# Performance work log

Measured on AMD Instinct MI355X. Metric: run time of the kernel, lower is better.

Reference implementation:

```python
import jax, jax.numpy as jnp
import numpy as np

M, N = 4096, 4096  # placement density grid size (even, as the rfft-based kernel assumes)


def _expk(L):
    # precompute_expk(L): [cos(pi*k/(2L)), sin(pi*k/(2L))] stacked -> [L, 2]
    a = np.pi * np.arange(L) / (2.0 * L)
    return np.stack([np.cos(a), np.sin(a)], axis=-1).astype(np.float32)


def setup_inputs() -> dict:
    key = jax.random.key(0)
    x = jax.random.normal(key, (M, N), dtype=jnp.float32)
    return {
        "x": x,
        "expkM": jnp.asarray(_expk(M)),
        "expkN": jnp.asarray(_expk(N)),
    }


def _idct1d(x, expk):
    # Unnormalized IDCT (DCT-III with DC weight 1) along the last axis:
    #   y_u = sum_k x_k * cos(pi*k*(2u+1)/(2L))
    # Makhoul FFT trick: c_k = x_k * exp(i*pi*k/(2L)); v = L*ifft(c);
    #   y[2m] = Re(v[m]),  y[2m+1] = Re(v[L-1-m])
    L = x.shape[-1]
    ek = expk[:, 0] + 1j * expk[:, 1]            # exp(i*pi*k/(2L)), [L]
    v = (jnp.fft.ifft(x * ek, axis=-1) * L).real  # [..., L]
    half = L // 2
    even = v[..., :half]                          # y[0], y[2], ...
    odd = v[..., ::-1][..., :half]                # y[1], y[3], ... (= v[L-1], v[L-2], ...)
    return jnp.stack([even, odd], axis=-1).reshape(x.shape)


def reference(x, expkM, expkN):
    # out[u,v] = sum_{p,q} x[p,q] cos(pi*p*(2u+1)/(2M)) cos(pi*q*(2v+1)/(2N))
    t = _idct1d(x, expkN)                               # transform along N (last dim)
    out = _idct1d(t.swapaxes(-1, -2), expkM)            # transform along M
    return out.swapaxes(-1, -2)
```

## Files before the change

### kernel.cpp

```cpp
#include <hip/hip_runtime.h>
#include <stdint.h>

typedef __bf16 bf16x8_t __attribute__((ext_vector_type(8)));
typedef float f32x4_t __attribute__((ext_vector_type(4)));

__device__ __forceinline__ uint32_t f32_to_bf16_bits(float f) {
    union { float f; uint32_t u; } v; v.f = f;
    return (v.u + 0x7FFFu + ((v.u >> 16) & 1u)) >> 16;
}

__global__ void prep_kernel(const float* __restrict__ X,
                            unsigned short* __restrict__ Ae,
                            unsigned short* __restrict__ Ao,
                            unsigned short* __restrict__ Xe,
                            unsigned short* __restrict__ Xo) {
    if (blockIdx.x < 4096) {
        const int idx = blockIdx.x * 256 + threadIdx.x;
        const int sel = idx >> 19;
        const int e   = idx & ((1 << 19) - 1);
        const int n   = e >> 8;
        const int c0  = (e & 255) << 3;
        const uint32_t tn = (uint32_t)(2 * n + 1);
        unsigned short* dst = sel ? Ao : Ae;
        uint32_t packed[4];
#pragma unroll
        for (int jj = 0; jj < 4; ++jj) {
            uint32_t cA = (uint32_t)(c0 + 2 * jj);
            uint32_t cB = cA + 1;
            uint32_t r0 = ((2u * cA + (uint32_t)sel) * tn) & 16383u;
            uint32_t r1 = ((2u * cB + (uint32_t)sel) * tn) & 16383u;
            float v0 = __cosf((float)r0 * 3.8349519697141e-4f);
            float v1 = __cosf((float)r1 * 3.8349519697141e-4f);
            packed[jj] = f32_to_bf16_bits(v0) | (f32_to_bf16_bits(v1) << 16);
        }
        *(uint4*)(dst + (size_t)n * 2048 + c0) = make_uint4(packed[0], packed[1], packed[2], packed[3]);
    } else {
        const int idx = (blockIdx.x - 4096) * 256 + threadIdx.x;
        const int q   = idx >> 9;
        const int p0  = (idx & 511) << 3;
        const float4* src = (const float4*)(X + (size_t)q * 4096 + p0);
        float4 a = src[0];
        float4 b = src[1];
        uint2 ev, od;
        ev.x = f32_to_bf16_bits(a.x) | (f32_to_bf16_bits(a.z) << 16);
        ev.y = f32_to_bf16_bits(b.x) | (f32_to_bf16_bits(b.z) << 16);
        od.x = f32_to_bf16_bits(a.y) | (f32_to_bf16_bits(a.w) << 16);
        od.y = f32_to_bf16_bits(b.y) | (f32_to_bf16_bits(b.w) << 16);
        *(uint2*)(Xe + (size_t)q * 2048 + (p0 >> 1)) = ev;
        *(uint2*)(Xo + (size_t)q * 2048 + (p0 >> 1)) = od;
    }
}

template <int STAGE>
__global__ __launch_bounds__(256, 2)
void gemm_fused_kernel(const unsigned short* __restrict__ Ae,
                       const unsigned short* __restrict__ Ao,
                       const unsigned short* __restrict__ Re,
                       const unsigned short* __restrict__ Ro,
                       unsigned short* __restrict__ Te,
                       unsigned short* __restrict__ To,
                       float* __restrict__ out) {
    constexpr int KD = 2048;
    constexpr int BK = 64;
    __shared__ __attribute__((aligned(16))) unsigned short lAe[128 * BK];
    __shared__ __attribute__((aligned(16))) unsigned short lAo[128 * BK];
    __shared__ __attribute__((aligned(16))) unsigned short lBe[128 * BK];
    __shared__ __attribute__((aligned(16))) unsigned short lBo[128 * BK];

    const int tid  = threadIdx.x;
    const int wave = tid >> 6;
    const int lane = tid & 63;

    const int tile_m = blockIdx.y << 7;
    const int tile_c = blockIdx.x << 7;

    f32x4_t acc_e[4][4], acc_o[4][4];
#pragma unroll
    for (int i = 0; i < 4; ++i)
#pragma unroll
        for (int j = 0; j < 4; ++j) {
            acc_e[i][j] = (f32x4_t){0.f, 0.f, 0.f, 0.f};
            acc_o[i][j] = (f32x4_t){0.f, 0.f, 0.f, 0.f};
        }

    const int c_base = wave << 6;
    size_t roff[4];
#pragma unroll
    for (int t = 0; t < 4; ++t) {
        const int cl   = c_base + lane + 256 * t;
        const int row  = cl >> 3;
        const int grp  = (cl & 7) ^ (row & 7);
        roff[t] = (size_t)row * KD + ((size_t)grp << 3);
    }

    const unsigned short* gAe = Ae + (size_t)tile_m * KD;
    const unsigned short* gAo = Ao + (size_t)tile_m * KD;
    const unsigned short* gBe = Re + (size_t)tile_c * KD;
    const unsigned short* gBo = Ro + (size_t)tile_c * KD;

    int lbase[4];
#pragma unroll
    for (int t = 0; t < 4; ++t) lbase[t] = (c_base + 256 * t) << 3;

    const int frow = lane & 15;
    const int sw   = frow & 7;
    const int gq   = lane >> 4;
    const int aRowB = ((wave >> 1) * 64 + frow) * BK;
    const int bRowB = ((wave & 1) * 64 + frow) * BK;

#define GLL(gp, lp) __builtin_amdgcn_global_load_lds( \
        (const __attribute__((address_space(1))) uint32_t*)(gp), \
        (__attribute__((address_space(3))) uint32_t*)(lp), 16, 0, 0)

    for (int kt = 0; kt < KD / BK; ++kt) {
        const size_t kadv = (size_t)kt * BK;
        __syncthreads();
#pragma unroll
        for (int t = 0; t < 4; ++t) {
            GLL(gAe + kadv + roff[t], &lAe[lbase[t]]);
            GLL(gAo + kadv + roff[t], &lAo[lbase[t]]);
            GLL(gBe + kadv + roff[t], &lBe[lbase[t]]);
            GLL(gBo + kadv + roff[t], &lBo[lbase[t]]);
        }
        __syncthreads();

#pragma unroll
        for (int kh = 0; kh < 2; ++kh) {
            const int slotOff = (((kh * 4 + gq) ^ sw) << 3);
            {
                bf16x8_t af[4], bfr[4];
#pragma unroll
                for (int i = 0; i < 4; ++i) af[i]  = *(const bf16x8_t*)(&lAe[aRowB + i * 16 * BK + slotOff]);
#pragma unroll
                for (int j = 0; j < 4; ++j) bfr[j] = *(const bf16x8_t*)(&lBe[bRowB + j * 16 * BK + slotOff]);
#pragma unroll
                for (int i = 0; i < 4; ++i)
#pragma unroll
                    for (int j = 0; j < 4; ++j)
                        acc_e[i][j] = __builtin_amdgcn_mfma_f32_16x16x32_bf16(af[i], bfr[j], acc_e[i][j], 0, 0, 0);
            }
            {
                bf16x8_t af[4], bfr[4];
#pragma unroll
                for (int i = 0; i < 4; ++i) af[i]  = *(const bf16x8_t*)(&lAo[aRowB + i * 16 * BK + slotOff]);
#pragma unroll
                for (int j = 0; j < 4; ++j) bfr[j] = *(const bf16x8_t*)(&lBo[bRowB + j * 16 * BK + slotOff]);
#pragma unroll
                for (int i = 0; i < 4; ++i)
#pragma unroll
                    for (int j = 0; j < 4; ++j)
                        acc_o[i][j] = __builtin_amdgcn_mfma_f32_16x16x32_bf16(af[i], bfr[j], acc_o[i][j], 0, 0, 0);
            }
        }
    }
#undef GLL

    const int orow = tile_m + (wave >> 1) * 64 + ((lane >> 4) << 2);
    const int ocol = tile_c + (wave & 1) * 64 + (lane & 15);
    if (STAGE == 1) {
        unsigned short* dst = (ocol & 1) ? To : Te;
#pragma unroll
        for (int i = 0; i < 4; ++i)
#pragma unroll
            for (int j = 0; j < 4; ++j)
#pragma unroll
                for (int r = 0; r < 4; ++r) {
                    const int n = orow + i * 16 + r;
                    const int c = (ocol + j * 16) >> 1;
                    const float e = acc_e[i][j][r], o = acc_o[i][j][r];
                    dst[(size_t)n * 2048 + c]          = (unsigned short)f32_to_bf16_bits(e + o);
                    dst[(size_t)(4095 - n) * 2048 + c] = (unsigned short)f32_to_bf16_bits(e - o);
                }
    } else {
#pragma unroll
        for (int i = 0; i < 4; ++i)
#pragma unroll
            for (int j = 0; j < 4; ++j)
#pragma unroll
                for (int r = 0; r < 4; ++r) {
                    const int m = orow + i * 16 + r;
                    const int w = ocol + j * 16;
                    const float e = acc_e[i][j][r], o = acc_o[i][j][r];
                    out[(size_t)m * 4096 + w]          = e + o;
                    out[(size_t)(4095 - m) * 4096 + w] = e - o;
                }
    }
}

extern "C" void kernel_launch(void* const* d_in, const int* in_sizes, int n_in,
                              void* d_out, int out_size, void* d_ws, size_t ws_size,
                              hipStream_t stream) {
    const float* x = (const float*)d_in[0];
    char* ws = (char*)d_ws;
    const size_t MB = 1024 * 1024;
    unsigned short* Ae = (unsigned short*)(ws);
    unsigned short* Ao = (unsigned short*)(ws + 8 * MB);
    unsigned short* Xe = (unsigned short*)(ws + 16 * MB);
    unsigned short* Xo = (unsigned short*)(ws + 32 * MB);
    unsigned short* Te = (unsigned short*)(ws + 48 * MB);
    unsigned short* To = (unsigned short*)(ws + 64 * MB);
    float* out = (float*)d_out;

    prep_kernel<<<12288, 256, 0, stream>>>(x, Ae, Ao, Xe, Xo);

    dim3 grid(32, 16);
    gemm_fused_kernel<1><<<grid, 256, 0, stream>>>(Ae, Ao, Xe, Xo, Te, To, nullptr);
    gemm_fused_kernel<2><<<grid, 256, 0, stream>>>(Ae, Ao, Te, To, nullptr, nullptr, out);
}
```

Before: 252.9 us.

## Triple-buffer LDS with interleaved async loads and 8-wave 128x256 tiles

```diff
diff --git a/kernel.cpp b/kernel.cpp
--- a/kernel.cpp
+++ b/kernel.cpp
@@ -51,8 +51,72 @@
     }
 }
 
+#define GLL(gp, lp) __builtin_amdgcn_global_load_lds( \
+        (const __attribute__((address_space(1))) uint32_t*)(gp), \
+        (__attribute__((address_space(3))) uint32_t*)(lp), 16, 0, 0)
+
+template <bool PRE, int VM>
+__device__ __forceinline__ void tile_step(f32x4_t (&acc)[4][4], const int t,
+        int& cur_off, int& stg_off, unsigned short* smem,
+        const unsigned short* pAe, const unsigned short* pAo,
+        const unsigned short* pBe, const unsigned short* pBo,
+        const int* a_src, const int* b_src, const int* a_lds, const int* b_lds,
+        const int aRow, const int bRow, const int gq, const int sw) {
+    const unsigned short* gA = pAe;
+    const unsigned short* gB = pBe;
+    size_t kadv = 0;
+    if (PRE) {
+        const int pre = t + 2;
+        gA = (pre < 32) ? pAe : pAo;
+        gB = (pre < 32) ? pBe : pBo;
+        kadv = (size_t)(pre & 31) << 6;
+    }
+    unsigned short* sA = smem + stg_off;
+    unsigned short* sB = sA + 8192;
+    const unsigned short* lA = smem + cur_off;
+    const unsigned short* lB = lA + 8192;
+
+#pragma unroll
+    for (int kh = 0; kh < 2; ++kh) {
+        const int so = (((kh << 2) + gq) ^ sw) << 3;
+        bf16x8_t af[4], bfr[4];
+#pragma unroll
+        for (int i = 0; i < 4; ++i) af[i]  = *(const bf16x8_t*)(lA + aRow + i * 1024 + so);
+#pragma unroll
+        for (int j = 0; j < 4; ++j) bfr[j] = *(const bf16x8_t*)(lB + bRow + j * 1024 + so);
+        if (PRE) {
+            if (kh == 0) {
+                GLL(gA + kadv + a_src[0], sA + a_lds[0]);
+                GLL(gB + kadv + b_src[0], sB + b_lds[0]);
+                GLL(gB + kadv + b_src[1], sB + b_lds[1]);
+            } else {
+                GLL(gA + kadv + a_src[1], sA + a_lds[1]);
+                GLL(gB + kadv + b_src[2], sB + b_lds[2]);
+                GLL(gB + kadv + b_src[3], sB + b_lds[3]);
+            }
+        }
+        asm volatile("" ::: "memory");
+        __builtin_amdgcn_s_barrier();
+        __builtin_amdgcn_s_setprio(1);
+#pragma unroll
+        for (int i = 0; i < 4; ++i)
+#pragma unroll
+            for (int j = 0; j < 4; ++j)
+                acc[i][j] = __builtin_amdgcn_mfma_f32_16x16x32_bf16(af[i], bfr[j], acc[i][j], 0, 0, 0);
+        __builtin_amdgcn_s_setprio(0);
+        if (kh == 1) {
+            if (VM == 6)      asm volatile("s_waitcnt vmcnt(6)" ::: "memory");
+            else if (VM == 0) asm volatile("s_waitcnt vmcnt(0)" ::: "memory");
+        }
+        asm volatile("" ::: "memory");
+        __builtin_amdgcn_s_barrier();
+    }
+    cur_off += 24576; if (cur_off == 73728) cur_off = 0;
+    stg_off += 24576; if (stg_off == 73728) stg_off = 0;
+}
+
 template <int STAGE>
-__global__ __launch_bounds__(256, 2)
+__global__ __launch_bounds__(512, 2)
 void gemm_fused_kernel(const unsigned short* __restrict__ Ae,
                        const unsigned short* __restrict__ Ao,
                        const unsigned short* __restrict__ Re,
@@ -61,18 +125,21 @@
                        unsigned short* __restrict__ To,
                        float* __restrict__ out) {
     constexpr int KD = 2048;
-    constexpr int BK = 64;
-    __shared__ __attribute__((aligned(16))) unsigned short lAe[128 * BK];
-    __shared__ __attribute__((aligned(16))) unsigned short lAo[128 * BK];
-    __shared__ __attribute__((aligned(16))) unsigned short lBe[128 * BK];
-    __shared__ __attribute__((aligned(16))) unsigned short lBo[128 * BK];
+    __shared__ __attribute__((aligned(16))) unsigned short smem[3 * 24576];
 
     const int tid  = threadIdx.x;
     const int wave = tid >> 6;
     const int lane = tid & 63;
-
-    const int tile_m = blockIdx.y << 7;
-    const int tile_c = blockIdx.x << 7;
+    const int wm   = wave >> 2;
+    const int wn   = wave & 3;
+
+    const int tile_n = blockIdx.y << 7;
+    const int tile_c = blockIdx.x << 8;
+
+    const unsigned short* pAe = Ae + (size_t)tile_n * KD;
+    const unsigned short* pAo = Ao + (size_t)tile_n * KD;
+    const unsigned short* pBe = Re + (size_t)tile_c * KD;
+    const unsigned short* pBo = Ro + (size_t)tile_c * KD;
 
     f32x4_t acc_e[4][4], acc_o[4][4];
 #pragma unroll
@@ -83,90 +150,73 @@
             acc_o[i][j] = (f32x4_t){0.f, 0.f, 0.f, 0.f};
         }
 
-    const int c_base = wave << 6;
-    size_t roff[4];
-#pragma unroll
-    for (int t = 0; t < 4; ++t) {
-        const int cl   = c_base + lane + 256 * t;
-        const int row  = cl >> 3;
-        const int grp  = (cl & 7) ^ (row & 7);
-        roff[t] = (size_t)row * KD + ((size_t)grp << 3);
-    }
-
-    const unsigned short* gAe = Ae + (size_t)tile_m * KD;
-    const unsigned short* gAo = Ao + (size_t)tile_m * KD;
-    const unsigned short* gBe = Re + (size_t)tile_c * KD;
-    const unsigned short* gBo = Ro + (size_t)tile_c * KD;
-
-    int lbase[4];
-#pragma unroll
-    for (int t = 0; t < 4; ++t) lbase[t] = (c_base + 256 * t) << 3;
+    int a_src[2], a_lds[2], b_src[4], b_lds[4];
+#pragma unroll
+    for (int k2 = 0; k2 < 2; ++k2) {
+        const int c = tid + 512 * k2, row = c >> 3, g = (c & 7) ^ (row & 7);
+        a_src[k2] = row * KD + g * 8;
+        a_lds[k2] = c * 8;
+    }
+#pragma unroll
+    for (int k2 = 0; k2 < 4; ++k2) {
+        const int c = tid + 512 * k2, row = c >> 3, g = (c & 7) ^ (row & 7);
+        b_src[k2] = row * KD + g * 8;
+        b_lds[k2] = c * 8;
+    }
 
     const int frow = lane & 15;
     const int sw   = frow & 7;
     const int gq   = lane >> 4;
-    const int aRowB = ((wave >> 1) * 64 + frow) * BK;
-    const int bRowB = ((wave & 1) * 64 + frow) * BK;
-
-#define GLL(gp, lp) __builtin_amdgcn_global_load_lds( \
-        (const __attribute__((address_space(1))) uint32_t*)(gp), \
-        (__attribute__((address_space(3))) uint32_t*)(lp), 16, 0, 0)
-
-    for (int kt = 0; kt < KD / BK; ++kt) {
-        const size_t kadv = (size_t)kt * BK;
-        __syncthreads();
-#pragma unroll
-        for (int t = 0; t < 4; ++t) {
-            GLL(gAe + kadv + roff[t], &lAe[lbase[t]]);
-            GLL(gAo + kadv + roff[t], &lAo[lbase[t]]);
-            GLL(gBe + kadv + roff[t], &lBe[lbase[t]]);
-            GLL(gBo + kadv + roff[t], &lBo[lbase[t]]);
-        }
-        __syncthreads();
-
-#pragma unroll
-        for (int kh = 0; kh < 2; ++kh) {
-            const int slotOff = (((kh * 4 + gq) ^ sw) << 3);
-            {
-                bf16x8_t af[4], bfr[4];
-#pragma unroll
-                for (int i = 0; i < 4; ++i) af[i]  = *(const bf16x8_t*)(&lAe[aRowB + i * 16 * BK + slotOff]);
-#pragma unroll
-                for (int j = 0; j < 4; ++j) bfr[j] = *(const bf16x8_t*)(&lBe[bRowB + j * 16 * BK + slotOff]);
-#pragma unroll
-                for (int i = 0; i < 4; ++i)
-#pragma unroll
-                    for (int j = 0; j < 4; ++j)
-                        acc_e[i][j] = __builtin_amdgcn_mfma_f32_16x16x32_bf16(af[i], bfr[j], acc_e[i][j], 0, 0, 0);
-            }
-            {
-                bf16x8_t af[4], bfr[4];
-#pragma unroll
-                for (int i = 0; i < 4; ++i) af[i]  = *(const bf16x8_t*)(&lAo[aRowB + i * 16 * BK + slotOff]);
-#pragma unroll
-                for (int j = 0; j < 4; ++j) bfr[j] = *(const bf16x8_t*)(&lBo[bRowB + j * 16 * BK + slotOff]);
-#pragma unroll
-                for (int i = 0; i < 4; ++i)
-#pragma unroll
-                    for (int j = 0; j < 4; ++j)
-                        acc_o[i][j] = __builtin_amdgcn_mfma_f32_16x16x32_bf16(af[i], bfr[j], acc_o[i][j], 0, 0, 0);
-            }
-        }
-    }
-#undef GLL
-
-    const int orow = tile_m + (wave >> 1) * 64 + ((lane >> 4) << 2);
-    const int ocol = tile_c + (wave & 1) * 64 + (lane & 15);
+    const int aRow = (wm * 64 + frow) * 64;
+    const int bRow = (wn * 64 + frow) * 64;
+
+    {
+        unsigned short* s0 = smem;
+        GLL(pAe + a_src[0], s0 + a_lds[0]);
+        GLL(pBe + b_src[0], s0 + 8192 + b_lds[0]);
+        GLL(pBe + b_src[1], s0 + 8192 + b_lds[1]);
+        GLL(pAe + a_src[1], s0 + a_lds[1]);
+        GLL(pBe + b_src[2], s0 + 8192 + b_lds[2]);
+        GLL(pBe + b_src[3], s0 + 8192 + b_lds[3]);
+        unsigned short* s1 = smem + 24576;
+        GLL(pAe + 64 + a_src[0], s1 + a_lds[0]);
+        GLL(pBe + 64 + b_src[0], s1 + 8192 + b_lds[0]);
+        GLL(pBe + 64 + b_src[1], s1 + 8192 + b_lds[1]);
+        GLL(pAe + 64 + a_src[1], s1 + a_lds[1]);
+        GLL(pBe + 64 + b_src[2], s1 + 8192 + b_lds[2]);
+        GLL(pBe + 64 + b_src[3], s1 + 8192 + b_lds[3]);
+        asm volatile("s_waitcnt vmcnt(6)" ::: "memory");
+        __builtin_amdgcn_s_barrier();
+    }
+
+    int cur_off = 0;
+    int stg_off = 49152;
+
+#pragma unroll 1
+    for (int t = 0; t < 32; ++t)
+        tile_step<true, 6>(acc_e, t, cur_off, stg_off, smem, pAe, pAo, pBe, pBo,
+                           a_src, b_src, a_lds, b_lds, aRow, bRow, gq, sw);
+#pragma unroll 1
+    for (int t = 32; t < 62; ++t)
+        tile_step<true, 6>(acc_o, t, cur_off, stg_off, smem, pAe, pAo, pBe, pBo,
+                           a_src, b_src, a_lds, b_lds, aRow, bRow, gq, sw);
+    tile_step<false, 0>(acc_o, 62, cur_off, stg_off, smem, pAe, pAo, pBe, pBo,
+                        a_src, b_src, a_lds, b_lds, aRow, bRow, gq, sw);
+    tile_step<false, -1>(acc_o, 63, cur_off, stg_off, smem, pAe, pAo, pBe, pBo,
+                         a_src, b_src, a_lds, b_lds, aRow, bRow, gq, sw);
+
+    const int orow0 = tile_n + wm * 64 + ((lane >> 4) << 2);
+    const int ocol0 = tile_c + wn * 64 + (lane & 15);
     if (STAGE == 1) {
-        unsigned short* dst = (ocol & 1) ? To : Te;
+        unsigned short* dst = (ocol0 & 1) ? To : Te;
 #pragma unroll
         for (int i = 0; i < 4; ++i)
 #pragma unroll
             for (int j = 0; j < 4; ++j)
 #pragma unroll
                 for (int r = 0; r < 4; ++r) {
-                    const int n = orow + i * 16 + r;
-                    const int c = (ocol + j * 16) >> 1;
+                    const int n = orow0 + i * 16 + r;
+                    const int c = (ocol0 + j * 16) >> 1;
                     const float e = acc_e[i][j][r], o = acc_o[i][j][r];
                     dst[(size_t)n * 2048 + c]          = (unsigned short)f32_to_bf16_bits(e + o);
                     dst[(size_t)(4095 - n) * 2048 + c] = (unsigned short)f32_to_bf16_bits(e - o);
@@ -178,8 +228,8 @@
             for (int j = 0; j < 4; ++j)
 #pragma unroll
                 for (int r = 0; r < 4; ++r) {
-                    const int m = orow + i * 16 + r;
-                    const int w = ocol + j * 16;
+                    const int m = orow0 + i * 16 + r;
+                    const int w = ocol0 + j * 16;
                     const float e = acc_e[i][j][r], o = acc_o[i][j][r];
                     out[(size_t)m * 4096 + w]          = e + o;
                     out[(size_t)(4095 - m) * 4096 + w] = e - o;
@@ -203,7 +253,7 @@
 
     prep_kernel<<<12288, 256, 0, stream>>>(x, Ae, Ao, Xe, Xo);
 
-    dim3 grid(32, 16);
-    gemm_fused_kernel<1><<<grid, 256, 0, stream>>>(Ae, Ao, Xe, Xo, Te, To, nullptr);
-    gemm_fused_kernel<2><<<grid, 256, 0, stream>>>(Ae, Ao, Te, To, nullptr, nullptr, out);
-}
+    dim3 grid(16, 16);
+    gemm_fused_kernel<1><<<grid, 512, 0, stream>>>(Ae, Ao, Xe, Xo, Te, To, nullptr);
+    gemm_fused_kernel<2><<<grid, 512, 0, stream>>>(Ae, Ao, Te, To, nullptr, nullptr, out);
+}
```

Measured after the change: 265.8 us. +5.1%, slower.

## Double-buffer LDS and stream even then odd K-phases to overlap loads with MFMA

Applied to the files above, without the earlier changes.

```diff
diff --git a/kernel.cpp b/kernel.cpp
--- a/kernel.cpp
+++ b/kernel.cpp
@@ -51,6 +51,45 @@
     }
 }
 
+#define GLL(gp, lp) __builtin_amdgcn_global_load_lds( \
+        (const __attribute__((address_space(1))) uint32_t*)(gp), \
+        (__attribute__((address_space(3))) uint32_t*)(lp), 16, 0, 0)
+
+#define STAGE8(buf, gA, gB, kadv) do {                                        \
+    _Pragma("unroll")                                                         \
+    for (int k_ = 0; k_ < 4; ++k_) {                                          \
+        GLL((gA) + (kadv) + src_off[k_], (buf) + uldsb[k_]);                  \
+        GLL((gB) + (kadv) + src_off[k_], (buf) + 8192 + uldsb[k_]);           \
+    }                                                                         \
+} while (0)
+
+#define COMPUTE_TILE(buf, acc) do {                                           \
+    const unsigned short* lA_ = (buf);                                        \
+    const unsigned short* lB_ = (buf) + 8192;                                 \
+    _Pragma("unroll")                                                         \
+    for (int kh_ = 0; kh_ < 2; ++kh_) {                                       \
+        const int so_ = (((kh_ << 2) + gq) ^ sw) << 3;                        \
+        bf16x8_t af_[4], bf_[4];                                              \
+        _Pragma("unroll")                                                     \
+        for (int i_ = 0; i_ < 4; ++i_) af_[i_] = *(const bf16x8_t*)(lA_ + aRow + i_ * 1024 + so_); \
+        _Pragma("unroll")                                                     \
+        for (int j_ = 0; j_ < 4; ++j_) bf_[j_] = *(const bf16x8_t*)(lB_ + bRow + j_ * 1024 + so_); \
+        __builtin_amdgcn_s_setprio(1);                                        \
+        _Pragma("unroll")                                                     \
+        for (int i_ = 0; i_ < 4; ++i_)                                        \
+            _Pragma("unroll")                                                 \
+            for (int j_ = 0; j_ < 4; ++j_)                                    \
+                acc[i_][j_] = __builtin_amdgcn_mfma_f32_16x16x32_bf16(af_[i_], bf_[j_], acc[i_][j_], 0, 0, 0); \
+        __builtin_amdgcn_s_setprio(0);                                        \
+    }                                                                         \
+} while (0)
+
+#define TILE_SYNC() do {                                                      \
+    asm volatile("s_waitcnt vmcnt(0)" ::: "memory");                          \
+    __builtin_amdgcn_s_barrier();                                             \
+    asm volatile("" ::: "memory");                                            \
+} while (0)
+
 template <int STAGE>
 __global__ __launch_bounds__(256, 2)
 void gemm_fused_kernel(const unsigned short* __restrict__ Ae,
@@ -61,11 +100,7 @@
                        unsigned short* __restrict__ To,
                        float* __restrict__ out) {
     constexpr int KD = 2048;
-    constexpr int BK = 64;
-    __shared__ __attribute__((aligned(16))) unsigned short lAe[128 * BK];
-    __shared__ __attribute__((aligned(16))) unsigned short lAo[128 * BK];
-    __shared__ __attribute__((aligned(16))) unsigned short lBe[128 * BK];
-    __shared__ __attribute__((aligned(16))) unsigned short lBo[128 * BK];
+    __shared__ __attribute__((aligned(16))) unsigned short smem[2 * 16384];
 
     const int tid  = threadIdx.x;
     const int wave = tid >> 6;
@@ -73,6 +108,11 @@
 
     const int tile_m = blockIdx.y << 7;
     const int tile_c = blockIdx.x << 7;
+
+    const unsigned short* pAe = Ae + (size_t)tile_m * KD;
+    const unsigned short* pAo = Ao + (size_t)tile_m * KD;
+    const unsigned short* pBe = Re + (size_t)tile_c * KD;
+    const unsigned short* pBo = Ro + (size_t)tile_c * KD;
 
     f32x4_t acc_e[4][4], acc_o[4][4];
 #pragma unroll
@@ -83,77 +123,45 @@
             acc_o[i][j] = (f32x4_t){0.f, 0.f, 0.f, 0.f};
         }
 
-    const int c_base = wave << 6;
-    size_t roff[4];
-#pragma unroll
-    for (int t = 0; t < 4; ++t) {
-        const int cl   = c_base + lane + 256 * t;
-        const int row  = cl >> 3;
-        const int grp  = (cl & 7) ^ (row & 7);
-        roff[t] = (size_t)row * KD + ((size_t)grp << 3);
-    }
-
-    const unsigned short* gAe = Ae + (size_t)tile_m * KD;
-    const unsigned short* gAo = Ao + (size_t)tile_m * KD;
-    const unsigned short* gBe = Re + (size_t)tile_c * KD;
-    const unsigned short* gBo = Ro + (size_t)tile_c * KD;
-
-    int lbase[4];
-#pragma unroll
-    for (int t = 0; t < 4; ++t) lbase[t] = (c_base + 256 * t) << 3;
+    int src_off[4], uldsb[4];
+#pragma unroll
+    for (int k = 0; k < 4; ++k) {
+        const int c   = (wave << 6) + lane + (k << 8);
+        const int row = c >> 3;
+        const int g   = (c & 7) ^ (row & 7);
+        src_off[k] = row * KD + (g << 3);
+        uldsb[k]   = ((wave << 6) + (k << 8)) << 3;
+    }
 
     const int frow = lane & 15;
     const int sw   = frow & 7;
     const int gq   = lane >> 4;
-    const int aRowB = ((wave >> 1) * 64 + frow) * BK;
-    const int bRowB = ((wave & 1) * 64 + frow) * BK;
-
-#define GLL(gp, lp) __builtin_amdgcn_global_load_lds( \
-        (const __attribute__((address_space(1))) uint32_t*)(gp), \
-        (__attribute__((address_space(3))) uint32_t*)(lp), 16, 0, 0)
-
-    for (int kt = 0; kt < KD / BK; ++kt) {
-        const size_t kadv = (size_t)kt * BK;
-        __syncthreads();
-#pragma unroll
-        for (int t = 0; t < 4; ++t) {
-            GLL(gAe + kadv + roff[t], &lAe[lbase[t]]);
-            GLL(gAo + kadv + roff[t], &lAo[lbase[t]]);
-            GLL(gBe + kadv + roff[t], &lBe[lbase[t]]);
-            GLL(gBo + kadv + roff[t], &lBo[lbase[t]]);
-        }
-        __syncthreads();
-
-#pragma unroll
-        for (int kh = 0; kh < 2; ++kh) {
-            const int slotOff = (((kh * 4 + gq) ^ sw) << 3);
-            {
-                bf16x8_t af[4], bfr[4];
-#pragma unroll
-                for (int i = 0; i < 4; ++i) af[i]  = *(const bf16x8_t*)(&lAe[aRowB + i * 16 * BK + slotOff]);
-#pragma unroll
-                for (int j = 0; j < 4; ++j) bfr[j] = *(const bf16x8_t*)(&lBe[bRowB + j * 16 * BK + slotOff]);
-#pragma unroll
-                for (int i = 0; i < 4; ++i)
-#pragma unroll
-                    for (int j = 0; j < 4; ++j)
-                        acc_e[i][j] = __builtin_amdgcn_mfma_f32_16x16x32_bf16(af[i], bfr[j], acc_e[i][j], 0, 0, 0);
-            }
-            {
-                bf16x8_t af[4], bfr[4];
-#pragma unroll
-                for (int i = 0; i < 4; ++i) af[i]  = *(const bf16x8_t*)(&lAo[aRowB + i * 16 * BK + slotOff]);
-#pragma unroll
-                for (int j = 0; j < 4; ++j) bfr[j] = *(const bf16x8_t*)(&lBo[bRowB + j * 16 * BK + slotOff]);
-#pragma unroll
-                for (int i = 0; i < 4; ++i)
-#pragma unroll
-                    for (int j = 0; j < 4; ++j)
-                        acc_o[i][j] = __builtin_amdgcn_mfma_f32_16x16x32_bf16(af[i], bfr[j], acc_o[i][j], 0, 0, 0);
-            }
-        }
-    }
-#undef GLL
+    const int aRow = ((wave >> 1) * 64 + frow) * 64;
+    const int bRow = ((wave & 1) * 64 + frow) * 64;
+
+    STAGE8(smem, pAe, pBe, 0);
+    TILE_SYNC();
+
+    int co = 0;
+#pragma unroll 1
+    for (int t = 0; t < 31; ++t) {
+        STAGE8(smem + (co ^ 16384), pAe, pBe, (size_t)(t + 1) << 6);
+        COMPUTE_TILE(smem + co, acc_e);
+        TILE_SYNC();
+        co ^= 16384;
+    }
+    STAGE8(smem + (co ^ 16384), pAo, pBo, 0);
+    COMPUTE_TILE(smem + co, acc_e);
+    TILE_SYNC();
+    co ^= 16384;
+#pragma unroll 1
+    for (int t = 0; t < 31; ++t) {
+        STAGE8(smem + (co ^ 16384), pAo, pBo, (size_t)(t + 1) << 6);
+        COMPUTE_TILE(smem + co, acc_o);
+        TILE_SYNC();
+        co ^= 16384;
+    }
+    COMPUTE_TILE(smem + co, acc_o);
 
     const int orow = tile_m + (wave >> 1) * 64 + ((lane >> 4) << 2);
     const int ocol = tile_c + (wave & 1) * 64 + (lane & 15);
```

After: 252.6 us, median of 3. About the same (-0.1%).
